# Performance work log

Measured on AMD Instinct MI355X. Metric: run time of the kernel, lower is better.

The kernel has to match this reference:

```python
import jax, jax.numpy as jnp
import numpy as np

T = 32            # num_tsteps
B = 8192          # batch_size
W_IN0, W_OUT0 = 36, 18
W_IN1, W_OUT1 = 18, 8
TILE0, TILE1 = 2, 1
BETA = (0.95, 0.95)
TH = (0.55, 0.25)
Q = 15000.0       # sephia mrr_Q
ER_DB = 20.0      # sephia extinction ratio
IL_DB = 0.0       # sephia insertion loss
SHIFT_PM = -250.0 # sephia resonance shift per unit spike
P_UNITY = 1e-4    # dbm_to_watt(-10): optical power per WDM channel at unit input


def _lif(inp, mem, beta, th):
    # snntorch Leaky, reset_mechanism='zero', reset_delay=True:
    # reset decided from incoming mem, membrane zeroed before leak+integrate.
    reset = (mem > th).astype(inp.dtype)
    mem_new = (beta * mem + inp) * (1.0 - reset)
    spk = (mem_new > th).astype(inp.dtype)
    return spk, mem_new


def _allpass(spk, wl_nm):
    # All-pass MRR modulator: spike shifts the ring resonance by SHIFT_PM.
    # Normalized detuning delta = shift / (FWHM/2), FWHM = lambda / Q.
    fwhm_pm = wl_nm * 1e3 / Q                      # [C]
    delta = (spk * SHIFT_PM) / (0.5 * fwhm_pm)     # [B, C]
    gamma = 10.0 ** (-ER_DB / 20.0)                # on-resonance amplitude (ER)
    il = 10.0 ** (-IL_DB / 20.0)                   # insertion loss factor
    return (il * (1j * delta + gamma) / (1j * delta + 1.0)).astype(jnp.complex64)


def setup_inputs() -> dict:
    key = jax.random.key(0)
    ks = jax.random.split(key, 6)
    return {
        "x_in": jax.random.uniform(ks[0], (T, B, W_IN0), jnp.float32),
        "W0": jax.random.uniform(ks[1], (TILE0, W_IN0 // TILE0, W_OUT0 * 2 // TILE0), jnp.float32),
        "d0": jax.random.normal(ks[2], (TILE0, W_OUT0 // TILE0), jnp.float32) * 5e3,
        "W1": jax.random.uniform(ks[3], (TILE1, W_IN1 // TILE1, W_OUT1 * 2 // TILE1), jnp.float32),
        "d1": jax.random.normal(ks[4], (TILE1, W_OUT1 // TILE1), jnp.float32) * 5e3,
        "peak_powers_dbm": jax.random.uniform(ks[5], (W_IN0,), jnp.float32, -15.0, -5.0),
    }


def reference(x_in, W0, d0, W1, d1, peak_powers_dbm):
    wl0 = 1550.0 + 0.8 * jnp.arange(W_OUT0, dtype=jnp.float32)   # MRR resonance wavelengths (nm)
    # sephia_inputs: sqrt(dbm_to_watt(P_dbm) * 1e6) field amplitude per channel
    amp0 = jnp.sqrt((10.0 ** (peak_powers_dbm[:W_OUT0] / 10.0) / 1000.0) * 1e6)
    S0 = W_OUT0 * 2 // TILE0   # 18 spatial channels after EO broadcast
    S1 = W_OUT1 * 2 // TILE1   # 16 spatial channels into layer 1

    def step(carry, x_t):
        mem0, mem1 = carry
        b = x_t.shape[0]
        # --- EO conversion + layer 0 MRR weight bank (power domain) ---
        p_in = x_t * P_UNITY                                     # [B, 36] optical power
        p0 = jnp.broadcast_to(p_in[:, :, None], (b, W_IN0, S0)).reshape(b, TILE0, W_IN0 // TILE0, S0)
        I0 = jnp.einsum('btws,tws->bts', p0, W0)                 # photocurrents [B,2,18]
        cur0 = ((I0[..., 0::2] - I0[..., 1::2]) * d0).reshape(b, W_OUT0)  # balanced PDs + Diagonal
        spk0, mem0 = _lif(cur0, mem0, BETA[0], TH[0])
        # --- SEPhIA all-pass MRR modulation of comb lines ---
        lo = _allpass(spk0, wl0) * amp0.astype(jnp.complex64)    # [B, 18] complex field
        pw0 = jnp.abs(lo) ** 2                                   # detected power == spike record
        # --- post-SEPhIA broadcast + layer 1 weight bank ---
        p1 = jnp.broadcast_to(pw0[:, :, None], (b, W_IN1, S1)).reshape(b, TILE1, W_IN1 // TILE1, S1)
        I1 = jnp.einsum('btws,tws->bts', p1, W1)                 # [B,1,16]
        cur1 = ((I1[..., 0::2] - I1[..., 1::2]) * d1).reshape(b, W_OUT1)
        spk1, mem1 = _lif(cur1, mem1, BETA[1], TH[1])
        return (mem0, mem1), (pw0, spk1, mem0, mem1)

    mem0 = jnp.zeros((x_in.shape[1], W_OUT0), x_in.dtype)
    mem1 = jnp.zeros((x_in.shape[1], W_OUT1), x_in.dtype)
    _, (spks0, spks1, mems0, mems1) = jax.lax.scan(step, (mem0, mem1), x_in)
    return spks0, spks1, mems0, mems1
```

## Files before the change

kernel.cpp:

```cpp
#include <hip/hip_runtime.h>


namespace {
constexpr int Tn = 32;
constexpr int Bn = 8192;
constexpr int O_PW = 0;
constexpr int O_S1 = Tn * Bn * 18;
constexpr int O_M0 = O_S1 + Tn * Bn * 8;
constexpr int O_M1 = O_M0 + Tn * Bn * 18;
}

__global__ __launch_bounds__(256, 1)
void oesnn_kernel(const float* __restrict__ x_in,
                  const float* __restrict__ W0g,
                  const float* __restrict__ d0g,
                  const float* __restrict__ W1g,
                  const float* __restrict__ d1g,
                  const float* __restrict__ peakg,
                  float* __restrict__ out)
{
    const int lt  = threadIdx.x & 63;
    const int tid = blockIdx.x * 256 + threadIdx.x;
    const int b   = tid >> 3;
    const int sub = tid & 7;
    const int tl  = sub >> 2;
    const int q   = sub & 3;
    const int j0  = (q == 0) ? 0 : (2 * q + 1);
    const int nj  = (q == 0) ? 3 : 2;

    float w0e[3][18], w0o[3][18], dd0[3], pon[3], poff[3];
    #pragma unroll
    for (int j = 0; j < 3; ++j) {
        const int jc = (j < nj) ? (j0 + j) : j0;
        dd0[j] = d0g[tl * 9 + jc];
        #pragma unroll
        for (int w = 0; w < 18; ++w) {
            const float2 p = *(const float2*)(W0g + ((tl * 18 + w) * 18 + 2 * jc));
            w0e[j][w] = p.x;
            w0o[j][w] = p.y;
        }
        const int c = tl * 9 + jc;
        const float wl    = 1550.0f + 0.8f * (float)c;
        const float halfw = 0.5f * (wl * 1e3f / 15000.0f);
        const float amp   = sqrtf((exp10f(peakg[c] / 10.0f) / 1000.0f) * 1e6f);
        {
            const float lr = 0.1f * amp;
            const float a  = sqrtf(lr * lr);
            poff[j] = a * a;
        }
        {
            const float delta = -250.0f / halfw;
            const float den = fmaf(delta, delta, 1.0f);
            const float qr  = fmaf(delta, delta, 0.1f) / den;
            const float qi  = (delta - 0.1f * delta) / den;
            const float lr = qr * amp, li = qi * amp;
            const float a  = sqrtf(fmaf(lr, lr, li * li));
            pon[j] = a * a;
        }
    }

    float w1e[18], w1o[18];
    #pragma unroll
    for (int w = 0; w < 18; ++w) {
        const float2 pp = *(const float2*)(W1g + w * 16 + 2 * sub);
        w1e[w] = pp.x;
        w1o[w] = pp.y;
    }
    const float dd1 = d1g[sub];

    float mem0[3] = {0.f, 0.f, 0.f};
    float mem1 = 0.f;

    const float* xp = x_in + (size_t)b * 36 + tl * 18;
    float* opw = out + O_PW + (size_t)b * 18 + tl * 9 + j0;
    float* om0 = out + O_M0 + (size_t)b * 18 + tl * 9 + j0;
    float* os1 = out + O_S1 + (size_t)b * 8 + sub;
    float* om1 = out + O_M1 + (size_t)b * 8 + sub;

    float2 xv[9];
    #pragma unroll
    for (int k = 0; k < 9; ++k) xv[k] = *(const float2*)(xp + 2 * k);

    const int basel = lt & ~7;

    #pragma unroll 1
    for (int t = 0; t < Tn; ++t) {
        float p[18];
        #pragma unroll
        for (int k = 0; k < 9; ++k) {
            p[2 * k]     = xv[k].x * 1e-4f;
            p[2 * k + 1] = xv[k].y * 1e-4f;
        }
        xp += Bn * 36;
        if (t < Tn - 1) {
            #pragma unroll
            for (int k = 0; k < 9; ++k) xv[k] = *(const float2*)(xp + 2 * k);
        }

        float pwv[3];
        #pragma unroll
        for (int j = 0; j < 3; ++j) {
            float se = 0.f, so = 0.f;
            #pragma unroll
            for (int w = 0; w < 18; ++w) {
                se = fmaf(p[w], w0e[j][w], se);
                so = fmaf(p[w], w0o[j][w], so);
            }
            const float c0 = (se - so) * dd0[j];
            const float m  = mem0[j];
            const float m2 = (m > 0.55f) ? 0.0f : fmaf(0.95f, m, c0);
            mem0[j] = m2;
            pwv[j]  = (m2 > 0.55f) ? pon[j] : poff[j];
        }

        #pragma unroll
        for (int j = 0; j < 3; ++j) {
            if (j < nj) {
                opw[j] = pwv[j];
                om0[j] = mem0[j];
            }
        }

        float pwall[18];
        #pragma unroll
        for (int c = 0; c < 18; ++c) {
            const int tlc = c / 9, jc2 = c % 9;
            const int qo  = (jc2 < 3) ? 0 : ((jc2 - 1) / 2);
            const int st  = (qo == 0) ? 0 : (2 * qo + 1);
            const int r   = jc2 - st;
            pwall[c] = __shfl(pwv[r], basel + tlc * 4 + qo, 64);
        }

        float i1e = 0.f, i1o = 0.f;
        #pragma unroll
        for (int w = 0; w < 18; ++w) {
            i1e = fmaf(pwall[w], w1e[w], i1e);
            i1o = fmaf(pwall[w], w1o[w], i1o);
        }

        const float c1 = (i1e - i1o) * dd1;
        const float m  = mem1;
        const float m2 = (m > 0.25f) ? 0.0f : fmaf(0.95f, m, c1);
        mem1 = m2;
        *os1 = (m2 > 0.25f) ? 1.0f : 0.0f;
        *om1 = m2;

        opw += Bn * 18;
        om0 += Bn * 18;
        os1 += Bn * 8;
        om1 += Bn * 8;
    }
}

extern "C" void kernel_launch(void* const* d_in, const int* in_sizes, int n_in,
                              void* d_out, int out_size, void* d_ws, size_t ws_size,
                              hipStream_t stream) {
    (void)in_sizes; (void)n_in; (void)out_size; (void)d_ws; (void)ws_size;
    const float* x  = (const float*)d_in[0];
    const float* W0 = (const float*)d_in[1];
    const float* d0 = (const float*)d_in[2];
    const float* W1 = (const float*)d_in[3];
    const float* d1 = (const float*)d_in[4];
    const float* pk = (const float*)d_in[5];
    float* out = (float*)d_out;

    dim3 grid(Bn * 8 / 256), block(256);
    hipLaunchKernelGGL(oesnn_kernel, grid, block, 0, stream,
                       x, W0, d0, W1, d1, pk, out);
}
```

Measured before the change: 118.0 us.

## Assign one thread per output neuron with 32 lanes per batch row

```diff
diff --git a/kernel.cpp b/kernel.cpp
--- a/kernel.cpp
+++ b/kernel.cpp
@@ -10,7 +10,7 @@
 constexpr int O_M1 = O_M0 + Tn * Bn * 18;
 }
 
-__global__ __launch_bounds__(256, 1)
+__global__ __launch_bounds__(256, 4)
 void oesnn_kernel(const float* __restrict__ x_in,
                   const float* __restrict__ W0g,
                   const float* __restrict__ d0g,
@@ -21,32 +21,33 @@
 {
     const int lt  = threadIdx.x & 63;
     const int tid = blockIdx.x * 256 + threadIdx.x;
-    const int b   = tid >> 3;
-    const int sub = tid & 7;
-    const int tl  = sub >> 2;
-    const int q   = sub & 3;
-    const int j0  = (q == 0) ? 0 : (2 * q + 1);
-    const int nj  = (q == 0) ? 3 : 2;
+    const int b   = tid >> 5;
+    const int g   = tid & 31;
+    const bool isL0 = (g < 18);
+    const bool isL1 = (g >= 18) && (g < 26);
 
-    float w0e[3][18], w0o[3][18], dd0[3], pon[3], poff[3];
-    #pragma unroll
-    for (int j = 0; j < 3; ++j) {
-        const int jc = (j < nj) ? (j0 + j) : j0;
-        dd0[j] = d0g[tl * 9 + jc];
+    float wA[18], wB[18];
+    float dd = 0.f, pon = 0.f, poff = 0.f;
+    int tl = 0;
+
+    if (isL0) {
+        tl = g / 9;
+        const int jc = g % 9;
+        dd = d0g[tl * 9 + jc];
         #pragma unroll
         for (int w = 0; w < 18; ++w) {
             const float2 p = *(const float2*)(W0g + ((tl * 18 + w) * 18 + 2 * jc));
-            w0e[j][w] = p.x;
-            w0o[j][w] = p.y;
+            wA[w] = p.x;
+            wB[w] = p.y;
         }
-        const int c = tl * 9 + jc;
+        const int c = g;
         const float wl    = 1550.0f + 0.8f * (float)c;
         const float halfw = 0.5f * (wl * 1e3f / 15000.0f);
         const float amp   = sqrtf((exp10f(peakg[c] / 10.0f) / 1000.0f) * 1e6f);
         {
             const float lr = 0.1f * amp;
             const float a  = sqrtf(lr * lr);
-            poff[j] = a * a;
+            poff = a * a;
         }
         {
             const float delta = -250.0f / halfw;
@@ -55,95 +56,79 @@
             const float qi  = (delta - 0.1f * delta) / den;
             const float lr = qr * amp, li = qi * amp;
             const float a  = sqrtf(fmaf(lr, lr, li * li));
-            pon[j] = a * a;
+            pon = a * a;
+        }
+    } else {
+        const int o = (g < 26) ? (g - 18) : 7;
+        dd = d1g[o];
+        #pragma unroll
+        for (int w = 0; w < 18; ++w) {
+            const float2 p = *(const float2*)(W1g + w * 16 + 2 * o);
+            wA[w] = p.x;
+            wB[w] = p.y;
         }
     }
 
-    float w1e[18], w1o[18];
-    #pragma unroll
-    for (int w = 0; w < 18; ++w) {
-        const float2 pp = *(const float2*)(W1g + w * 16 + 2 * sub);
-        w1e[w] = pp.x;
-        w1o[w] = pp.y;
-    }
-    const float dd1 = d1g[sub];
-
-    float mem0[3] = {0.f, 0.f, 0.f};
+    float mem0 = 0.f;
     float mem1 = 0.f;
 
     const float* xp = x_in + (size_t)b * 36 + tl * 18;
-    float* opw = out + O_PW + (size_t)b * 18 + tl * 9 + j0;
-    float* om0 = out + O_M0 + (size_t)b * 18 + tl * 9 + j0;
-    float* os1 = out + O_S1 + (size_t)b * 8 + sub;
-    float* om1 = out + O_M1 + (size_t)b * 8 + sub;
+    float* opw = out + O_PW + (size_t)b * 18 + g;
+    float* om0 = out + O_M0 + (size_t)b * 18 + g;
+    const int o1 = isL1 ? (g - 18) : 0;
+    float* os1 = out + O_S1 + (size_t)b * 8 + o1;
+    float* om1 = out + O_M1 + (size_t)b * 8 + o1;
 
     float2 xv[9];
     #pragma unroll
     for (int k = 0; k < 9; ++k) xv[k] = *(const float2*)(xp + 2 * k);
 
-    const int basel = lt & ~7;
+    const int basel = lt & ~31;
 
     #pragma unroll 1
     for (int t = 0; t < Tn; ++t) {
-        float p[18];
+        float se = 0.f, so = 0.f;
         #pragma unroll
         for (int k = 0; k < 9; ++k) {
-            p[2 * k]     = xv[k].x * 1e-4f;
-            p[2 * k + 1] = xv[k].y * 1e-4f;
+            const float pa = xv[k].x * 1e-4f;
+            se = fmaf(pa, wA[2 * k], se);
+            so = fmaf(pa, wB[2 * k], so);
+            const float pb = xv[k].y * 1e-4f;
+            se = fmaf(pb, wA[2 * k + 1], se);
+            so = fmaf(pb, wB[2 * k + 1], so);
         }
+
         xp += Bn * 36;
         if (t < Tn - 1) {
             #pragma unroll
             for (int k = 0; k < 9; ++k) xv[k] = *(const float2*)(xp + 2 * k);
         }
 
-        float pwv[3];
-        #pragma unroll
-        for (int j = 0; j < 3; ++j) {
-            float se = 0.f, so = 0.f;
-            #pragma unroll
-            for (int w = 0; w < 18; ++w) {
-                se = fmaf(p[w], w0e[j][w], se);
-                so = fmaf(p[w], w0o[j][w], so);
-            }
-            const float c0 = (se - so) * dd0[j];
-            const float m  = mem0[j];
-            const float m2 = (m > 0.55f) ? 0.0f : fmaf(0.95f, m, c0);
-            mem0[j] = m2;
-            pwv[j]  = (m2 > 0.55f) ? pon[j] : poff[j];
-        }
+        const float c0 = (se - so) * dd;
+        const float m2 = (mem0 > 0.55f) ? 0.0f : fmaf(0.95f, mem0, c0);
+        mem0 = m2;
+        const float pw = (m2 > 0.55f) ? pon : poff;
 
-        #pragma unroll
-        for (int j = 0; j < 3; ++j) {
-            if (j < nj) {
-                opw[j] = pwv[j];
-                om0[j] = mem0[j];
-            }
-        }
-
-        float pwall[18];
-        #pragma unroll
-        for (int c = 0; c < 18; ++c) {
-            const int tlc = c / 9, jc2 = c % 9;
-            const int qo  = (jc2 < 3) ? 0 : ((jc2 - 1) / 2);
-            const int st  = (qo == 0) ? 0 : (2 * qo + 1);
-            const int r   = jc2 - st;
-            pwall[c] = __shfl(pwv[r], basel + tlc * 4 + qo, 64);
+        if (isL0) {
+            *opw = pw;
+            *om0 = m2;
         }
 
         float i1e = 0.f, i1o = 0.f;
         #pragma unroll
-        for (int w = 0; w < 18; ++w) {
-            i1e = fmaf(pwall[w], w1e[w], i1e);
-            i1o = fmaf(pwall[w], w1o[w], i1o);
+        for (int c = 0; c < 18; ++c) {
+            const float gp = __shfl(pw, basel + c, 64);
+            i1e = fmaf(gp, wA[c], i1e);
+            i1o = fmaf(gp, wB[c], i1o);
         }
 
-        const float c1 = (i1e - i1o) * dd1;
-        const float m  = mem1;
-        const float m2 = (m > 0.25f) ? 0.0f : fmaf(0.95f, m, c1);
-        mem1 = m2;
-        *os1 = (m2 > 0.25f) ? 1.0f : 0.0f;
-        *om1 = m2;
+        const float c1 = (i1e - i1o) * dd;
+        const float m3 = (mem1 > 0.25f) ? 0.0f : fmaf(0.95f, mem1, c1);
+        mem1 = m3;
+        if (isL1) {
+            *os1 = (m3 > 0.25f) ? 1.0f : 0.0f;
+            *om1 = m3;
+        }
 
         opw += Bn * 18;
         om0 += Bn * 18;
@@ -164,7 +149,7 @@
     const float* pk = (const float*)d_in[5];
     float* out = (float*)d_out;
 
-    dim3 grid(Bn * 8 / 256), block(256);
+    dim3 grid(Bn * 32 / 256), block(256);
     hipLaunchKernelGGL(oesnn_kernel, grid, block, 0, stream,
                        x, W0, d0, W1, d1, pk, out);
 }
```

Measured after the change: 135.6 us. 1.15x slower.

## Stage weights in LDS and prefetch inputs four timesteps ahead

Applied to the files above, without the earlier changes.

```diff
diff --git a/kernel.cpp b/kernel.cpp
--- a/kernel.cpp
+++ b/kernel.cpp
@@ -28,17 +28,26 @@
     const int j0  = (q == 0) ? 0 : (2 * q + 1);
     const int nj  = (q == 0) ? 3 : 2;
 
-    float w0e[3][18], w0o[3][18], dd0[3], pon[3], poff[3];
+    __shared__ float4 lw0[2][9][9];
+    __shared__ float4 lw1[8][9];
+    if (threadIdx.x < 162) {
+        const int tl_ = threadIdx.x / 81;
+        const int r   = threadIdx.x % 81;
+        const int jc_ = r / 9, k_ = r % 9;
+        const float* base = W0g + ((size_t)(tl_ * 18 + 2 * k_) * 18) + 2 * jc_;
+        lw0[tl_][jc_][k_] = make_float4(base[0], base[1], base[18], base[19]);
+    } else if (threadIdx.x < 234) {
+        const int i  = threadIdx.x - 162;
+        const int o_ = i / 9, k_ = i % 9;
+        const float* base = W1g + (size_t)(2 * k_) * 16 + 2 * o_;
+        lw1[o_][k_] = make_float4(base[0], base[1], base[16], base[17]);
+    }
+
+    float dd0[3], pon[3], poff[3];
     #pragma unroll
     for (int j = 0; j < 3; ++j) {
         const int jc = (j < nj) ? (j0 + j) : j0;
         dd0[j] = d0g[tl * 9 + jc];
-        #pragma unroll
-        for (int w = 0; w < 18; ++w) {
-            const float2 p = *(const float2*)(W0g + ((tl * 18 + w) * 18 + 2 * jc));
-            w0e[j][w] = p.x;
-            w0o[j][w] = p.y;
-        }
         const int c = tl * 9 + jc;
         const float wl    = 1550.0f + 0.8f * (float)c;
         const float halfw = 0.5f * (wl * 1e3f / 15000.0f);
@@ -58,53 +67,58 @@
             pon[j] = a * a;
         }
     }
+    const float dd1 = d1g[sub];
 
-    float w1e[18], w1o[18];
-    #pragma unroll
-    for (int w = 0; w < 18; ++w) {
-        const float2 pp = *(const float2*)(W1g + w * 16 + 2 * sub);
-        w1e[w] = pp.x;
-        w1o[w] = pp.y;
-    }
-    const float dd1 = d1g[sub];
+    __syncthreads();
 
     float mem0[3] = {0.f, 0.f, 0.f};
     float mem1 = 0.f;
 
-    const float* xp = x_in + (size_t)b * 36 + tl * 18;
+    const float* xb = x_in + (size_t)b * 36 + tl * 18;
     float* opw = out + O_PW + (size_t)b * 18 + tl * 9 + j0;
     float* om0 = out + O_M0 + (size_t)b * 18 + tl * 9 + j0;
     float* os1 = out + O_S1 + (size_t)b * 8 + sub;
     float* om1 = out + O_M1 + (size_t)b * 8 + sub;
 
-    float2 xv[9];
-    #pragma unroll
-    for (int k = 0; k < 9; ++k) xv[k] = *(const float2*)(xp + 2 * k);
-
     const int basel = lt & ~7;
 
-    #pragma unroll 1
-    for (int t = 0; t < Tn; ++t) {
+    float2 xv0[9], xv1[9], xv2[9], xv3[9];
+    {
+        const float2* s0 = (const float2*)(xb);
+        const float2* s1 = (const float2*)(xb + (size_t)1 * Bn * 36);
+        const float2* s2 = (const float2*)(xb + (size_t)2 * Bn * 36);
+        const float2* s3 = (const float2*)(xb + (size_t)3 * Bn * 36);
+        #pragma unroll
+        for (int k = 0; k < 9; ++k) { xv0[k] = s0[k]; xv1[k] = s1[k]; }
+        #pragma unroll
+        for (int k = 0; k < 9; ++k) { xv2[k] = s2[k]; xv3[k] = s3[k]; }
+    }
+
+    auto body = [&](float2 (&xv)[9], int tcur) {
         float p[18];
         #pragma unroll
         for (int k = 0; k < 9; ++k) {
             p[2 * k]     = xv[k].x * 1e-4f;
             p[2 * k + 1] = xv[k].y * 1e-4f;
         }
-        xp += Bn * 36;
-        if (t < Tn - 1) {
+        if (tcur + 4 < Tn) {
+            const float2* s = (const float2*)(xb + (size_t)(tcur + 4) * Bn * 36);
             #pragma unroll
-            for (int k = 0; k < 9; ++k) xv[k] = *(const float2*)(xp + 2 * k);
+            for (int k = 0; k < 9; ++k) xv[k] = s[k];
         }
 
         float pwv[3];
         #pragma unroll
         for (int j = 0; j < 3; ++j) {
+            const int jc = (j < nj) ? (j0 + j) : j0;
             float se = 0.f, so = 0.f;
             #pragma unroll
-            for (int w = 0; w < 18; ++w) {
-                se = fmaf(p[w], w0e[j][w], se);
-                so = fmaf(p[w], w0o[j][w], so);
+            for (int k = 0; k < 9; ++k) {
+                const float4 wv = lw0[tl][jc][k];
+                se = fmaf(p[2 * k],     wv.x, se);
+                so = fmaf(p[2 * k],     wv.y, so);
+                se = fmaf(p[2 * k + 1], wv.z, se);
+                so = fmaf(p[2 * k + 1], wv.w, so);
             }
             const float c0 = (se - so) * dd0[j];
             const float m  = mem0[j];
@@ -133,9 +147,12 @@
 
         float i1e = 0.f, i1o = 0.f;
         #pragma unroll
-        for (int w = 0; w < 18; ++w) {
-            i1e = fmaf(pwall[w], w1e[w], i1e);
-            i1o = fmaf(pwall[w], w1o[w], i1o);
+        for (int k = 0; k < 9; ++k) {
+            const float4 wv = lw1[sub][k];
+            i1e = fmaf(pwall[2 * k],     wv.x, i1e);
+            i1o = fmaf(pwall[2 * k],     wv.y, i1o);
+            i1e = fmaf(pwall[2 * k + 1], wv.z, i1e);
+            i1o = fmaf(pwall[2 * k + 1], wv.w, i1o);
         }
 
         const float c1 = (i1e - i1o) * dd1;
@@ -149,6 +166,14 @@
         om0 += Bn * 18;
         os1 += Bn * 8;
         om1 += Bn * 8;
+    };
+
+    #pragma unroll 1
+    for (int t = 0; t < Tn; t += 4) {
+        body(xv0, t);
+        body(xv1, t + 1);
+        body(xv2, t + 2);
+        body(xv3, t + 3);
     }
 }
 
```

New measurement: 117.9 us. Within noise of the previous version (-0.1%).

## Split even/odd photodetector sums across thread pairs to double thread count

Applied to the files above, without the earlier changes.

```diff
diff --git a/kernel.cpp b/kernel.cpp
--- a/kernel.cpp
+++ b/kernel.cpp
@@ -10,7 +10,7 @@
 constexpr int O_M1 = O_M0 + Tn * Bn * 18;
 }
 
-__global__ __launch_bounds__(256, 1)
+__global__ __launch_bounds__(256, 2)
 void oesnn_kernel(const float* __restrict__ x_in,
                   const float* __restrict__ W0g,
                   const float* __restrict__ d0g,
@@ -21,24 +21,24 @@
 {
     const int lt  = threadIdx.x & 63;
     const int tid = blockIdx.x * 256 + threadIdx.x;
-    const int b   = tid >> 3;
-    const int sub = tid & 7;
+    const int b   = tid >> 4;
+    const int h   = tid & 15;
+    const int sub = h >> 1;
+    const int par = h & 1;
     const int tl  = sub >> 2;
     const int q   = sub & 3;
     const int j0  = (q == 0) ? 0 : (2 * q + 1);
     const int nj  = (q == 0) ? 3 : 2;
 
-    float w0e[3][18], w0o[3][18], dd0[3], pon[3], poff[3];
+    float ww[3][18], w1[18];
+    float dd0[3], pon[3], poff[3];
     #pragma unroll
     for (int j = 0; j < 3; ++j) {
         const int jc = (j < nj) ? (j0 + j) : j0;
         dd0[j] = d0g[tl * 9 + jc];
         #pragma unroll
-        for (int w = 0; w < 18; ++w) {
-            const float2 p = *(const float2*)(W0g + ((tl * 18 + w) * 18 + 2 * jc));
-            w0e[j][w] = p.x;
-            w0o[j][w] = p.y;
-        }
+        for (int w = 0; w < 18; ++w)
+            ww[j][w] = W0g[(tl * 18 + w) * 18 + 2 * jc + par];
         const int c = tl * 9 + jc;
         const float wl    = 1550.0f + 0.8f * (float)c;
         const float halfw = 0.5f * (wl * 1e3f / 15000.0f);
@@ -58,14 +58,9 @@
             pon[j] = a * a;
         }
     }
-
-    float w1e[18], w1o[18];
     #pragma unroll
-    for (int w = 0; w < 18; ++w) {
-        const float2 pp = *(const float2*)(W1g + w * 16 + 2 * sub);
-        w1e[w] = pp.x;
-        w1o[w] = pp.y;
-    }
+    for (int w = 0; w < 18; ++w)
+        w1[w] = W1g[w * 16 + 2 * sub + par];
     const float dd1 = d1g[sub];
 
     float mem0[3] = {0.f, 0.f, 0.f};
@@ -81,7 +76,7 @@
     #pragma unroll
     for (int k = 0; k < 9; ++k) xv[k] = *(const float2*)(xp + 2 * k);
 
-    const int basel = lt & ~7;
+    const int base16 = lt & ~15;
 
     #pragma unroll 1
     for (int t = 0; t < Tn; ++t) {
@@ -100,12 +95,13 @@
         float pwv[3];
         #pragma unroll
         for (int j = 0; j < 3; ++j) {
-            float se = 0.f, so = 0.f;
+            float s = 0.f;
             #pragma unroll
-            for (int w = 0; w < 18; ++w) {
-                se = fmaf(p[w], w0e[j][w], se);
-                so = fmaf(p[w], w0o[j][w], so);
-            }
+            for (int w = 0; w < 18; ++w)
+                s = fmaf(p[w], ww[j][w], s);
+            const float o = __shfl_xor(s, 1, 64);
+            const float se = par ? o : s;
+            const float so = par ? s : o;
             const float c0 = (se - so) * dd0[j];
             const float m  = mem0[j];
             const float m2 = (m > 0.55f) ? 0.0f : fmaf(0.95f, m, c0);
@@ -116,34 +112,30 @@
         #pragma unroll
         for (int j = 0; j < 3; ++j) {
             if (j < nj) {
-                opw[j] = pwv[j];
-                om0[j] = mem0[j];
+                if (par == 0) opw[j] = pwv[j];
+                else          om0[j] = mem0[j];
             }
         }
 
-        float pwall[18];
+        float i1 = 0.f;
         #pragma unroll
         for (int c = 0; c < 18; ++c) {
             const int tlc = c / 9, jc2 = c % 9;
             const int qo  = (jc2 < 3) ? 0 : ((jc2 - 1) / 2);
             const int st  = (qo == 0) ? 0 : (2 * qo + 1);
             const int r   = jc2 - st;
-            pwall[c] = __shfl(pwv[r], basel + tlc * 4 + qo, 64);
+            const float gp = __shfl(pwv[r], base16 + 2 * (tlc * 4 + qo), 64);
+            i1 = fmaf(gp, w1[c], i1);
         }
-
-        float i1e = 0.f, i1o = 0.f;
-        #pragma unroll
-        for (int w = 0; w < 18; ++w) {
-            i1e = fmaf(pwall[w], w1e[w], i1e);
-            i1o = fmaf(pwall[w], w1o[w], i1o);
-        }
-
+        const float oi = __shfl_xor(i1, 1, 64);
+        const float i1e = par ? oi : i1;
+        const float i1o = par ? i1 : oi;
         const float c1 = (i1e - i1o) * dd1;
         const float m  = mem1;
-        const float m2 = (m > 0.25f) ? 0.0f : fmaf(0.95f, m, c1);
-        mem1 = m2;
-        *os1 = (m2 > 0.25f) ? 1.0f : 0.0f;
-        *om1 = m2;
+        const float m3 = (m > 0.25f) ? 0.0f : fmaf(0.95f, m, c1);
+        mem1 = m3;
+        if (par == 0) *os1 = (m3 > 0.25f) ? 1.0f : 0.0f;
+        else          *om1 = m3;
 
         opw += Bn * 18;
         om0 += Bn * 18;
@@ -164,7 +156,7 @@
     const float* pk = (const float*)d_in[5];
     float* out = (float*)d_out;
 
-    dim3 grid(Bn * 8 / 256), block(256);
+    dim3 grid(Bn * 16 / 256), block(256);
     hipLaunchKernelGGL(oesnn_kernel, grid, block, 0, stream,
                        x, W0, d0, W1, d1, pk, out);
 }
```

Result: slower. 127.7 us (+8.2%).
